# Optimization experiments

Hardware: AMD Instinct MI355X
Metric: run time of the kernel (lower is better)

The kernel has to match this reference:

```python
import jax, jax.numpy as jnp
import numpy as np

D, NH, NL, NP, DFF = 256, 8, 4, 4, 1024
HD = D // NH
SHAPES = np.array([[64, 64], [32, 32], [16, 16], [8, 8]], dtype=np.int32)  # (H, W) per level


def _layer_norm(x, g, b, eps=1e-5):
    mu = jnp.mean(x, -1, keepdims=True)
    var = jnp.mean((x - mu) ** 2, -1, keepdims=True)
    return (x - mu) * jax.lax.rsqrt(var + eps) * g + b


def _bilinear_sample(value_l, loc):
    # value_l: (N, H, W, NH, HD); loc: (N, Lq, NH, NP, 2) normalized to [0,1]
    # Matches F.grid_sample(align_corners=False, padding_mode='zeros') on grid 2*loc-1.
    N, H, W = value_l.shape[0], value_l.shape[1], value_l.shape[2]
    x = loc[..., 0] * W - 0.5
    y = loc[..., 1] * H - 0.5
    x0 = jnp.floor(x)
    y0 = jnp.floor(y)
    wx1 = x - x0
    wy1 = y - y0
    b_idx = jnp.arange(N)[:, None, None, None]
    h_idx = jnp.arange(NH)[None, None, :, None]

    def gather(yi, xi):
        valid = (yi >= 0) & (yi < H) & (xi >= 0) & (xi < W)
        yc = jnp.clip(yi, 0, H - 1).astype(jnp.int32)
        xc = jnp.clip(xi, 0, W - 1).astype(jnp.int32)
        v = value_l[b_idx, yc, xc, h_idx]  # (N, Lq, NH, NP, HD)
        return v * valid[..., None].astype(value_l.dtype)

    v00 = gather(y0, x0)
    v01 = gather(y0, x0 + 1)
    v10 = gather(y0 + 1, x0)
    v11 = gather(y0 + 1, x0 + 1)
    wx1 = wx1[..., None]
    wy1 = wy1[..., None]
    top = v00 * (1 - wx1) + v01 * wx1
    bot = v10 * (1 - wx1) + v11 * wx1
    return top * (1 - wy1) + bot * wy1  # (N, Lq, NH, NP, HD)


def setup_inputs() -> dict:
    key = jax.random.key(0)
    ks = jax.random.split(key, 24)
    N, Lq = 8, int(SHAPES.prod(axis=1).sum())  # 5440
    s = 0.02
    return {
        "src": jax.random.normal(ks[0], (N, Lq, D), jnp.float32),
        "pos": jax.random.normal(ks[1], (N, Lq, D), jnp.float32),
        "reference_points": jax.random.uniform(ks[2], (N, Lq, NL, 2), jnp.float32),
        "spatial_shapes": jnp.asarray(SHAPES),
        "W_value": s * jax.random.normal(ks[3], (D, D)),
        "b_value": jnp.zeros((D,)),
        "W_off": s * jax.random.normal(ks[4], (D, NH * NL * NP * 2)),
        "b_off": 0.5 * jax.random.normal(ks[5], (NH * NL * NP * 2,)),
        "W_attn": s * jax.random.normal(ks[6], (D, NH * NL * NP)),
        "b_attn": jnp.zeros((NH * NL * NP,)),
        "W_out": s * jax.random.normal(ks[7], (D, D)),
        "b_out": jnp.zeros((D,)),
        "ln1_g": jnp.ones((D,)),
        "ln1_b": jnp.zeros((D,)),
        "W1": s * jax.random.normal(ks[8], (D, DFF)),
        "b1": jnp.zeros((DFF,)),
        "W2": s * jax.random.normal(ks[9], (DFF, D)),
        "b2": jnp.zeros((D,)),
        "ln2_g": jnp.ones((D,)),
        "ln2_b": jnp.zeros((D,)),
    }


def reference(src, pos, reference_points, spatial_shapes,
              W_value, b_value, W_off, b_off, W_attn, b_attn, W_out, b_out,
              ln1_g, ln1_b, W1, b1, W2, b2, ln2_g, ln2_b):
    shapes = np.asarray(spatial_shapes)  # static (NL, 2)
    N, Lq = src.shape[0], src.shape[1]

    # --- MSDeformAttn ---
    query = src + pos
    value = (src @ W_value + b_value).reshape(N, Lq, NH, HD)
    offsets = (query @ W_off + b_off).reshape(N, Lq, NH, NL, NP, 2)
    attn = jax.nn.softmax((query @ W_attn + b_attn).reshape(N, Lq, NH, NL * NP), axis=-1)
    attn = attn.reshape(N, Lq, NH, NL, NP)
    # offset normalizer is (W, H) per level
    norm = jnp.asarray(np.stack([shapes[:, 1], shapes[:, 0]], -1), jnp.float32)  # (NL, 2)
    loc = reference_points[:, :, None, :, None, :] + offsets / norm[None, None, None, :, None, :]

    out = jnp.zeros((N, Lq, NH, HD), src.dtype)
    start = 0
    for l in range(NL):
        H, W = int(shapes[l, 0]), int(shapes[l, 1])
        v_l = jax.lax.dynamic_slice_in_dim(value, start, H * W, axis=1).reshape(N, H, W, NH, HD)
        sampled = _bilinear_sample(v_l, loc[:, :, :, l])  # (N, Lq, NH, NP, HD)
        out = out + jnp.einsum('nqhp,nqhpd->nqhd', attn[:, :, :, l], sampled)
        start += H * W
    src2 = out.reshape(N, Lq, D) @ W_out + b_out

    # --- residual + norm + FFN (dropout=0, eval) ---
    x = _layer_norm(src + src2, ln1_g, ln1_b)
    ffn = jax.nn.relu(x @ W1 + b1) @ W2 + b2
    return _layer_norm(x + ffn, ln2_g, ln2_b)
```

## Files before the change

### kernel.cpp

```cpp
#include <hip/hip_runtime.h>
#include <math.h>

#define LQ_ 5440
#define NB_ 8
#define NQ_ (NB_ * LQ_)
#define D_  256
#define NH_ 8
#define HD_ 32

typedef __attribute__((ext_vector_type(8))) short short8;
typedef __attribute__((ext_vector_type(4))) float f32x4;

__device__ __forceinline__ ushort f2bf(float f) {
    union { float f; unsigned u; } v; v.f = f;
    unsigned u = v.u;
    unsigned r = (u + 0x7FFFu + ((u >> 16) & 1u)) >> 16;
    return (ushort)r;
}

__device__ __forceinline__ void gload_lds16(const void* g, void* l) {
    __builtin_amdgcn_global_load_lds(
        (const __attribute__((address_space(1))) void*)g,
        (__attribute__((address_space(3))) void*)l, 16, 0, 0);
}

__device__ __forceinline__ void wg_barrier() {
    __builtin_amdgcn_sched_barrier(0);
    __builtin_amdgcn_s_barrier();
    __builtin_amdgcn_sched_barrier(0);
}

#define TPREP_ 736

__global__ __launch_bounds__(256)
void prep(const float* __restrict__ src, const float* __restrict__ pos,
          ushort* __restrict__ s_bf, ushort* __restrict__ q_bf,
          const float* __restrict__ Wv, const float* __restrict__ Woff,
          const float* __restrict__ Wattn, const float* __restrict__ Wout,
          const float* __restrict__ W1, const float* __restrict__ W2,
          ushort* __restrict__ Wv_t, ushort* __restrict__ Woff_t,
          ushort* __restrict__ Wattn_t, ushort* __restrict__ Wout_t,
          ushort* __restrict__ W1_t, ushort* __restrict__ W2_t) {
    __shared__ float tile[32][33];
    const int bid = blockIdx.x;
    const int tid = threadIdx.x;

    if (bid >= TPREP_) {
        const int i = (bid - TPREP_) * 256 + tid;
        const float4 s = ((const float4*)src)[i];
        const float4 p = ((const float4*)pos)[i];
        ushort4 a, b;
        a.x = f2bf(s.x); a.y = f2bf(s.y); a.z = f2bf(s.z); a.w = f2bf(s.w);
        b.x = f2bf(s.x + p.x); b.y = f2bf(s.y + p.y);
        b.z = f2bf(s.z + p.z); b.w = f2bf(s.w + p.w);
        ((ushort4*)s_bf)[i] = a;
        ((ushort4*)q_bf)[i] = b;
        return;
    }

    const float* W; ushort* Wt; int K, N, bx, by;
    if (bid < 64)       { W = Wv;    Wt = Wv_t;    K = 256;  N = 256;  bx = bid % 8;         by = bid / 8; }
    else if (bid < 128) { W = Woff;  Wt = Woff_t;  K = 256;  N = 256;  bx = (bid-64) % 8;    by = (bid-64) / 8; }
    else if (bid < 160) { W = Wattn; Wt = Wattn_t; K = 256;  N = 128;  bx = (bid-128) % 4;   by = (bid-128) / 4; }
    else if (bid < 224) { W = Wout;  Wt = Wout_t;  K = 256;  N = 256;  bx = (bid-160) % 8;   by = (bid-160) / 8; }
    else if (bid < 480) { W = W1;    Wt = W1_t;    K = 256;  N = 1024; bx = (bid-224) % 32;  by = (bid-224) / 32; }
    else                { W = W2;    Wt = W2_t;    K = 1024; N = 256;  bx = (bid-480) % 8;   by = (bid-480) / 8; }

    const int tx = tid & 31;
    const int ty = tid >> 5;
    for (int i = ty; i < 32; i += 8)
        tile[i][tx] = W[(size_t)(by * 32 + i) * N + bx * 32 + tx];
    __syncthreads();
    for (int i = ty; i < 32; i += 8)
        Wt[(size_t)(bx * 32 + i) * K + by * 32 + tx] = f2bf(tile[tx][i]);
}

#define BM 128
#define BN 128
#define BK 64

__global__ __launch_bounds__(256)
void mfma_gemm(const ushort* __restrict__ A, const ushort* __restrict__ Bt,
               const float* __restrict__ bias, float* __restrict__ Cf,
               ushort* __restrict__ Cb, int N, int K, int relu) {
    __shared__ ushort lA[2][BM * BK];
    __shared__ ushort lB[2][BN * BK];
    const int t = threadIdx.x;

    const int nt   = gridDim.x;
    const int nwg  = nt * gridDim.y;
    const int flat = blockIdx.y * nt + blockIdx.x;
    const int xc   = flat & 7;
    const int sl   = flat >> 3;
    const int q8   = nwg >> 3;
    const int rm8  = nwg & 7;
    const int wi   = (xc < rm8 ? xc * (q8 + 1) : rm8 * (q8 + 1) + (xc - rm8) * q8) + sl;
    const int col0 = (wi % nt) * BN;
    const int row0 = (wi / nt) * BM;

    const int w    = t >> 6;
    const int lr   = t & 15;
    const int quad = (t >> 4) & 3;
    const int wm   = (w >> 1) * 64;
    const int wn   = (w & 1) * 64;

    f32x4 acc[4][4];
    #pragma unroll
    for (int i = 0; i < 4; ++i)
        #pragma unroll
        for (int j = 0; j < 4; ++j)
            acc[i][j] = (f32x4){0.f, 0.f, 0.f, 0.f};

    const int sr = t >> 3;
    const int sc = (t & 7) * 8;
    const size_t aoff = (size_t)(row0 + sr) * K + sc;
    const size_t boff = (size_t)(col0 + sr) * K + sc;
    const int wb = w * 1024;

    auto stage = [&](int buf, int k0) {
        char* la = (char*)lA[buf] + wb;
        char* lb = (char*)lB[buf] + wb;
        #pragma unroll
        for (int g = 0; g < 4; ++g) {
            gload_lds16(A  + aoff + k0 + (size_t)g * 32 * K, la + g * 4096);
            gload_lds16(Bt + boff + k0 + (size_t)g * 32 * K, lb + g * 4096);
        }
    };

    stage(0, 0);
    int cur = 0;
    for (int k0 = 0; k0 < K; k0 += BK) {
        if (k0 + BK < K) {
            stage(cur ^ 1, k0 + BK);
            asm volatile("s_waitcnt vmcnt(8)" ::: "memory");
        } else {
            asm volatile("s_waitcnt vmcnt(0)" ::: "memory");
        }
        wg_barrier();
        const ushort* pA = lA[cur];
        const ushort* pB = lB[cur];
        #pragma unroll
        for (int kk = 0; kk < 2; ++kk) {
            short8 af[4], bfr[4];
            #pragma unroll
            for (int i = 0; i < 4; ++i)
                af[i] = *(const short8*)(pA + (wm + i * 16 + lr) * BK + kk * 32 + quad * 8);
            #pragma unroll
            for (int j = 0; j < 4; ++j)
                bfr[j] = *(const short8*)(pB + (wn + j * 16 + lr) * BK + kk * 32 + quad * 8);
            #pragma unroll
            for (int i = 0; i < 4; ++i)
                #pragma unroll
                for (int j = 0; j < 4; ++j)
                    acc[i][j] = __builtin_amdgcn_mfma_f32_16x16x32_bf16(af[i], bfr[j], acc[i][j], 0, 0, 0);
        }
        wg_barrier();
        cur ^= 1;
    }

    #pragma unroll
    for (int j = 0; j < 4; ++j) {
        const int col = col0 + wn + j * 16 + lr;
        const float bb = bias ? bias[col] : 0.f;
        #pragma unroll
        for (int i = 0; i < 4; ++i) {
            const int rbase = row0 + wm + i * 16 + quad * 4;
            #pragma unroll
            for (int r = 0; r < 4; ++r) {
                float v = acc[i][j][r] + bb;
                if (relu) v = fmaxf(v, 0.f);
                if (Cf) Cf[(size_t)(rbase + r) * N + col] = v;
                else    Cb[(size_t)(rbase + r) * N + col] = f2bf(v);
            }
        }
    }
}

__global__ __launch_bounds__(256)
void msda_sample(const ushort* __restrict__ value, const float* __restrict__ comb,
                 const float* __restrict__ b_off, const float* __restrict__ b_attn,
                 const float* __restrict__ refp, ushort* __restrict__ out) {
    __shared__ int s_blob[2048];
    int*   s_addr = s_blob;
    float* s_w    = (float*)(s_blob + 1024);

    const int t   = threadIdx.x;
    const int tq  = t >> 7;
    const int u   = t & 127;
    const int bid = blockIdx.x;
    const int swz = (bid & 7) * (NQ_ / 2 / 8) + (bid >> 3);
    const int nq  = swz * 2 + tq;
    const int n   = nq / LQ_;

    {
        const int h = u >> 4;
        const int p = u & 15;
        const int l = p >> 2;

        const int starts[4] = {0, 4096, 5120, 5376};
        const int Wl = 64 >> l;

        float a = comb[(size_t)nq * 384 + 256 + u] + b_attn[u];
        float m = a;
        #pragma unroll
        for (int o = 8; o > 0; o >>= 1) m = fmaxf(m, __shfl_xor(m, o));
        float e = __expf(a - m);
        float s = e;
        #pragma unroll
        for (int o = 8; o > 0; o >>= 1) s += __shfl_xor(s, o);
        const float wgt = e / s;

        const float rx = refp[(size_t)nq * 8 + l * 2 + 0];
        const float ry = refp[(size_t)nq * 8 + l * 2 + 1];
        const float ox = comb[(size_t)nq * 384 + u * 2 + 0] + b_off[u * 2 + 0];
        const float oy = comb[(size_t)nq * 384 + u * 2 + 1] + b_off[u * 2 + 1];

        const float fw = (float)Wl;
        const float x  = (rx + ox / fw) * fw - 0.5f;
        const float y  = (ry + oy / fw) * fw - 0.5f;
        const float x0f = floorf(x), y0f = floorf(y);
        const int   x0 = (int)x0f, y0 = (int)y0f;
        const float wx1 = x - x0f, wy1 = y - y0f;
        const float wx0 = 1.f - wx1, wy0 = 1.f - wy1;

        const float xm0 = (x0 >= 0 && x0 < Wl) ? 1.f : 0.f;
        const float xm1 = (x0 + 1 >= 0 && x0 + 1 < Wl) ? 1.f : 0.f;
        const float ym0 = (y0 >= 0 && y0 < Wl) ? 1.f : 0.f;
        const float ym1 = (y0 + 1 >= 0 && y0 + 1 < Wl) ? 1.f : 0.f;

        const int x0c = min(max(x0, 0), Wl - 1);
        const int x1c = min(max(x0 + 1, 0), Wl - 1);
        const int y0c = min(max(y0, 0), Wl - 1);
        const int y1c = min(max(y0 + 1, 0), Wl - 1);

        const int base = (n * LQ_ + starts[l]) * 512 + h * 64;
        const int idx  = (tq << 7) + (p << 3) + (h ^ (p & 7));
        s_addr[idx * 4 + 0] = base + (y0c * Wl + x0c) * 512;
        s_addr[idx * 4 + 1] = base + (y0c * Wl + x1c) * 512;
        s_addr[idx * 4 + 2] = base + (y1c * Wl + x0c) * 512;
        s_addr[idx * 4 + 3] = base + (y1c * Wl + x1c) * 512;
        s_w[idx * 4 + 0] = wgt * wy0 * wx0 * ym0 * xm0;
        s_w[idx * 4 + 1] = wgt * wy0 * wx1 * ym0 * xm1;
        s_w[idx * 4 + 2] = wgt * wy1 * wx0 * ym1 * xm0;
        s_w[idx * 4 + 3] = wgt * wy1 * wx1 * ym1 * xm1;
    }
    __syncthreads();

    {
        const int h   = u >> 4;
        const int d2  = u & 15;
        const int tqb = tq << 7;
        const uint dby = (uint)(d2 * 4);
        const char* vbase = (const char*)value;

        float acc0 = 0.f, acc1 = 0.f;
        #pragma unroll 8
        for (int p = 0; p < 16; ++p) {
            const int row = tqb + (p << 3) + (h ^ (p & 7));
            const int*   ap = s_addr + row * 4;
            const float* wp = s_w    + row * 4;
            #pragma unroll
            for (int c = 0; c < 4; ++c) {
                const uint v = *(const uint*)(vbase + ((uint)ap[c] + dby));
                const float w = wp[c];
                union { uint u; float f; } lo, hi;
                lo.u = v << 16;
                hi.u = v & 0xffff0000u;
                acc0 = fmaf(lo.f, w, acc0);
                acc1 = fmaf(hi.f, w, acc1);
            }
        }
        const uint packed = (uint)f2bf(acc0) | ((uint)f2bf(acc1) << 16);
        ((uint*)out)[(size_t)nq * 128 + u] = packed;
    }
}

__global__ __launch_bounds__(256)
void add_ln(const float* __restrict__ a, const float* __restrict__ b,
            const float* __restrict__ g, const float* __restrict__ be,
            float* __restrict__ xf, ushort* __restrict__ xb) {
    const int row  = blockIdx.x * 4 + (threadIdx.x >> 6);
    const int lane = threadIdx.x & 63;
    const size_t base = (size_t)row * 256 + lane * 4;

    const float4 av = *(const float4*)(a + base);
    const float4 bv = *(const float4*)(b + base);
    float4 x;
    x.x = av.x + bv.x; x.y = av.y + bv.y; x.z = av.z + bv.z; x.w = av.w + bv.w;

    float s = x.x + x.y + x.z + x.w;
    #pragma unroll
    for (int o = 32; o > 0; o >>= 1) s += __shfl_xor(s, o);
    const float mu = s * (1.f / 256.f);

    float4 dx;
    dx.x = x.x - mu; dx.y = x.y - mu; dx.z = x.z - mu; dx.w = x.w - mu;
    float vv = dx.x * dx.x + dx.y * dx.y + dx.z * dx.z + dx.w * dx.w;
    #pragma unroll
    for (int o = 32; o > 0; o >>= 1) vv += __shfl_xor(vv, o);
    const float rstd = rsqrtf(vv * (1.f / 256.f) + 1e-5f);

    const float4 gv  = *(const float4*)(g  + lane * 4);
    const float4 bev = *(const float4*)(be + lane * 4);
    float4 y;
    y.x = dx.x * rstd * gv.x + bev.x;
    y.y = dx.y * rstd * gv.y + bev.y;
    y.z = dx.z * rstd * gv.z + bev.z;
    y.w = dx.w * rstd * gv.w + bev.w;

    *(float4*)(xf + base) = y;
    if (xb) {
        ushort4 yb;
        yb.x = f2bf(y.x); yb.y = f2bf(y.y); yb.z = f2bf(y.z); yb.w = f2bf(y.w);
        *(ushort4*)(xb + base) = yb;
    }
}

extern "C" void kernel_launch(void* const* d_in, const int* in_sizes, int n_in,
                              void* d_out, int out_size, void* d_ws, size_t ws_size,
                              hipStream_t stream) {
    const float* src     = (const float*)d_in[0];
    const float* pos     = (const float*)d_in[1];
    const float* refp    = (const float*)d_in[2];
    const float* W_value = (const float*)d_in[4];
    const float* b_value = (const float*)d_in[5];
    const float* W_off   = (const float*)d_in[6];
    const float* b_off   = (const float*)d_in[7];
    const float* W_attn  = (const float*)d_in[8];
    const float* b_attn  = (const float*)d_in[9];
    const float* W_out   = (const float*)d_in[10];
    const float* b_out   = (const float*)d_in[11];
    const float* ln1g    = (const float*)d_in[12];
    const float* ln1b    = (const float*)d_in[13];
    const float* W1      = (const float*)d_in[14];
    const float* b1      = (const float*)d_in[15];
    const float* W2      = (const float*)d_in[16];
    const float* b2      = (const float*)d_in[17];
    const float* ln2g    = (const float*)d_in[18];
    const float* ln2b    = (const float*)d_in[19];
    float* out = (float*)d_out;
    char*  ws  = (char*)d_ws;

    const size_t SZ_BF = (size_t)NQ_ * 256 * 2;
    const size_t SZ_F  = (size_t)NQ_ * 256 * 4;
    ushort* s_bf    = (ushort*)(ws);
    ushort* q_bf    = (ushort*)(ws + SZ_BF);
    ushort* val_bf  = (ushort*)(ws + 2 * SZ_BF);
    float*  comb    = (float*) (ws + 3 * SZ_BF);
    ushort* samp_bf = (ushort*)(ws + 4 * SZ_BF + SZ_F);
    ushort* h_bf    = (ushort*)(ws);
    ushort* x_bf    = (ushort*)(ws + 3 * SZ_BF + SZ_F);
    char*   wbase   = ws + 5 * SZ_BF + SZ_F;
    ushort* Wv_t    = (ushort*)(wbase);
    ushort* Woff_t  = (ushort*)(wbase + 131072);
    ushort* Wattn_t = (ushort*)(wbase + 262144);
    ushort* Wout_t  = (ushort*)(wbase + 327680);
    ushort* W1_t    = (ushort*)(wbase + 458752);
    ushort* W2_t    = (ushort*)(wbase + 983040);
    char*   fbase   = wbase + 1507328;
    float*  src2    = (float*)(fbase);
    float*  xf      = (float*)(fbase + SZ_F);

    prep<<<dim3(TPREP_ + (NQ_ * 256 / 4) / 256), 256, 0, stream>>>(
        src, pos, s_bf, q_bf, W_value, W_off, W_attn, W_out, W1, W2,
        Wv_t, Woff_t, Wattn_t, Wout_t, W1_t, W2_t);

    const int MT = NQ_ / BM;

    mfma_gemm<<<dim3(2, MT), 256, 0, stream>>>(s_bf, Wv_t, b_value, nullptr, val_bf, 256, 256, 0);
    mfma_gemm<<<dim3(3, MT), 256, 0, stream>>>(q_bf, Woff_t, nullptr, comb, nullptr, 384, 256, 0);
    msda_sample<<<dim3(NQ_ / 2), 256, 0, stream>>>(val_bf, comb, b_off, b_attn, refp, samp_bf);
    mfma_gemm<<<dim3(2, MT), 256, 0, stream>>>(samp_bf, Wout_t, b_out, src2, nullptr, 256, 256, 0);
    add_ln<<<dim3(NQ_ / 4), 256, 0, stream>>>(src, src2, ln1g, ln1b, xf, x_bf);
    mfma_gemm<<<dim3(8, MT), 256, 0, stream>>>(x_bf, W1_t, b1, nullptr, h_bf, 1024, 256, 1);
    mfma_gemm<<<dim3(2, MT), 256, 0, stream>>>(h_bf, W2_t, b2, src2, nullptr, 256, 1024, 0);
    add_ln<<<dim3(NQ_ / 4), 256, 0, stream>>>(xf, src2, ln2g, ln2b, out, nullptr);
}
```

Baseline: 487.8 us.

## Fuse value and offset/attn GEMMs into one launch with bf16 comb output

Merges the value projection and the offset/attention projection GEMMs into a single grid, where each block picks its problem from its column index. This removes one launch and balances tail blocks across both GEMMs. The combined offset/attention output is now stored as bf16 instead of fp32, halving its write and read traffic; offsets are now rounded to bf16, which costs some sampling-location precision. The sampler's LDS layout also drops the XOR swizzle for plain per-thread indexing, which may add bank conflicts.

```diff
diff --git a/kernel.cpp b/kernel.cpp
--- a/kernel.cpp
+++ b/kernel.cpp
@@ -16,6 +16,9 @@
     unsigned u = v.u;
     unsigned r = (u + 0x7FFFu + ((u >> 16) & 1u)) >> 16;
     return (ushort)r;
+}
+__device__ __forceinline__ float bf2f(ushort u) {
+    union { unsigned u; float f; } v; v.u = ((unsigned)u) << 16; return v.f;
 }
 
 __device__ __forceinline__ void gload_lds16(const void* g, void* l) {
@@ -79,25 +82,12 @@
 #define BN 128
 #define BK 64
 
-__global__ __launch_bounds__(256)
-void mfma_gemm(const ushort* __restrict__ A, const ushort* __restrict__ Bt,
-               const float* __restrict__ bias, float* __restrict__ Cf,
-               ushort* __restrict__ Cb, int N, int K, int relu) {
-    __shared__ ushort lA[2][BM * BK];
-    __shared__ ushort lB[2][BN * BK];
-    const int t = threadIdx.x;
-
-    const int nt   = gridDim.x;
-    const int nwg  = nt * gridDim.y;
-    const int flat = blockIdx.y * nt + blockIdx.x;
-    const int xc   = flat & 7;
-    const int sl   = flat >> 3;
-    const int q8   = nwg >> 3;
-    const int rm8  = nwg & 7;
-    const int wi   = (xc < rm8 ? xc * (q8 + 1) : rm8 * (q8 + 1) + (xc - rm8) * q8) + sl;
-    const int col0 = (wi % nt) * BN;
-    const int row0 = (wi / nt) * BM;
-
+__device__ __forceinline__ void gemm_body(
+    ushort* __restrict__ lAb, ushort* __restrict__ lBb,
+    const ushort* __restrict__ A, const ushort* __restrict__ Bt,
+    const float* __restrict__ bias, float* __restrict__ Cf,
+    ushort* __restrict__ Cb, int N, int K, int relu, int col0, int row0) {
+    const int t    = threadIdx.x;
     const int w    = t >> 6;
     const int lr   = t & 15;
     const int quad = (t >> 4) & 3;
@@ -118,8 +108,8 @@
     const int wb = w * 1024;
 
     auto stage = [&](int buf, int k0) {
-        char* la = (char*)lA[buf] + wb;
-        char* lb = (char*)lB[buf] + wb;
+        char* la = (char*)(lAb + buf * (BM * BK)) + wb;
+        char* lb = (char*)(lBb + buf * (BN * BK)) + wb;
         #pragma unroll
         for (int g = 0; g < 4; ++g) {
             gload_lds16(A  + aoff + k0 + (size_t)g * 32 * K, la + g * 4096);
@@ -137,8 +127,8 @@
             asm volatile("s_waitcnt vmcnt(0)" ::: "memory");
         }
         wg_barrier();
-        const ushort* pA = lA[cur];
-        const ushort* pB = lB[cur];
+        const ushort* pA = lAb + cur * (BM * BK);
+        const ushort* pB = lBb + cur * (BN * BK);
         #pragma unroll
         for (int kk = 0; kk < 2; ++kk) {
             short8 af[4], bfr[4];
@@ -177,12 +167,53 @@
 }
 
 __global__ __launch_bounds__(256)
-void msda_sample(const ushort* __restrict__ value, const float* __restrict__ comb,
+void mfma_gemm(const ushort* __restrict__ A, const ushort* __restrict__ Bt,
+               const float* __restrict__ bias, float* __restrict__ Cf,
+               ushort* __restrict__ Cb, int N, int K, int relu) {
+    __shared__ ushort lA[2][BM * BK];
+    __shared__ ushort lB[2][BN * BK];
+    const int nt   = gridDim.x;
+    const int nwg  = nt * gridDim.y;
+    const int flat = blockIdx.y * nt + blockIdx.x;
+    const int xc   = flat & 7;
+    const int sl   = flat >> 3;
+    const int q8   = nwg >> 3;
+    const int rm8  = nwg & 7;
+    const int wi   = (xc < rm8 ? xc * (q8 + 1) : rm8 * (q8 + 1) + (xc - rm8) * q8) + sl;
+    gemm_body(&lA[0][0], &lB[0][0], A, Bt, bias, Cf, Cb, N, K, relu,
+              (wi % nt) * BN, (wi / nt) * BM);
+}
+
+__global__ __launch_bounds__(256)
+void gemm_vc(const ushort* __restrict__ s_bf, const ushort* __restrict__ q_bf,
+             const ushort* __restrict__ Wv_t, const ushort* __restrict__ Woff_t,
+             const float* __restrict__ b_value,
+             ushort* __restrict__ val_bf, ushort* __restrict__ comb_bf) {
+    __shared__ ushort lA[2][BM * BK];
+    __shared__ ushort lB[2][BN * BK];
+    const int nwg  = gridDim.x;
+    const int flat = blockIdx.x;
+    const int xc   = flat & 7;
+    const int sl   = flat >> 3;
+    const int q8   = nwg >> 3;
+    const int rm8  = nwg & 7;
+    const int wi   = (xc < rm8 ? xc * (q8 + 1) : rm8 * (q8 + 1) + (xc - rm8) * q8) + sl;
+    const int ci   = wi % 5;
+    const int row0 = (wi / 5) * BM;
+    if (ci < 2)
+        gemm_body(&lA[0][0], &lB[0][0], s_bf, Wv_t, b_value, nullptr, val_bf,
+                  256, 256, 0, ci * BN, row0);
+    else
+        gemm_body(&lA[0][0], &lB[0][0], q_bf, Woff_t, nullptr, nullptr, comb_bf,
+                  384, 256, 0, (ci - 2) * BN, row0);
+}
+
+__global__ __launch_bounds__(256)
+void msda_sample(const ushort* __restrict__ value, const ushort* __restrict__ comb,
                  const float* __restrict__ b_off, const float* __restrict__ b_attn,
                  const float* __restrict__ refp, ushort* __restrict__ out) {
-    __shared__ int s_blob[2048];
-    int*   s_addr = s_blob;
-    float* s_w    = (float*)(s_blob + 1024);
+    __shared__ int   s_addr[256][4];
+    __shared__ float s_w[256][4];
 
     const int t   = threadIdx.x;
     const int tq  = t >> 7;
@@ -200,7 +231,7 @@
         const int starts[4] = {0, 4096, 5120, 5376};
         const int Wl = 64 >> l;
 
-        float a = comb[(size_t)nq * 384 + 256 + u] + b_attn[u];
+        float a = bf2f(comb[(size_t)nq * 384 + 256 + u]) + b_attn[u];
         float m = a;
         #pragma unroll
         for (int o = 8; o > 0; o >>= 1) m = fmaxf(m, __shfl_xor(m, o));
@@ -212,8 +243,9 @@
 
         const float rx = refp[(size_t)nq * 8 + l * 2 + 0];
         const float ry = refp[(size_t)nq * 8 + l * 2 + 1];
-        const float ox = comb[(size_t)nq * 384 + u * 2 + 0] + b_off[u * 2 + 0];
-        const float oy = comb[(size_t)nq * 384 + u * 2 + 1] + b_off[u * 2 + 1];
+        const uint  opk = *(const uint*)(comb + (size_t)nq * 384 + u * 2);
+        const float ox = bf2f((ushort)(opk & 0xffffu))  + b_off[u * 2 + 0];
+        const float oy = bf2f((ushort)(opk >> 16))      + b_off[u * 2 + 1];
 
         const float fw = (float)Wl;
         const float x  = (rx + ox / fw) * fw - 0.5f;
@@ -234,31 +266,29 @@
         const int y1c = min(max(y0 + 1, 0), Wl - 1);
 
         const int base = (n * LQ_ + starts[l]) * 512 + h * 64;
-        const int idx  = (tq << 7) + (p << 3) + (h ^ (p & 7));
-        s_addr[idx * 4 + 0] = base + (y0c * Wl + x0c) * 512;
-        s_addr[idx * 4 + 1] = base + (y0c * Wl + x1c) * 512;
-        s_addr[idx * 4 + 2] = base + (y1c * Wl + x0c) * 512;
-        s_addr[idx * 4 + 3] = base + (y1c * Wl + x1c) * 512;
-        s_w[idx * 4 + 0] = wgt * wy0 * wx0 * ym0 * xm0;
-        s_w[idx * 4 + 1] = wgt * wy0 * wx1 * ym0 * xm1;
-        s_w[idx * 4 + 2] = wgt * wy1 * wx0 * ym1 * xm0;
-        s_w[idx * 4 + 3] = wgt * wy1 * wx1 * ym1 * xm1;
+        s_addr[t][0] = base + (y0c * Wl + x0c) * 512;
+        s_addr[t][1] = base + (y0c * Wl + x1c) * 512;
+        s_addr[t][2] = base + (y1c * Wl + x0c) * 512;
+        s_addr[t][3] = base + (y1c * Wl + x1c) * 512;
+        s_w[t][0] = wgt * wy0 * wx0 * ym0 * xm0;
+        s_w[t][1] = wgt * wy0 * wx1 * ym0 * xm1;
+        s_w[t][2] = wgt * wy1 * wx0 * ym1 * xm0;
+        s_w[t][3] = wgt * wy1 * wx1 * ym1 * xm1;
     }
     __syncthreads();
 
     {
         const int h   = u >> 4;
         const int d2  = u & 15;
-        const int tqb = tq << 7;
+        const int sb  = tq * 128 + h * 16;
         const uint dby = (uint)(d2 * 4);
         const char* vbase = (const char*)value;
 
         float acc0 = 0.f, acc1 = 0.f;
         #pragma unroll 8
         for (int p = 0; p < 16; ++p) {
-            const int row = tqb + (p << 3) + (h ^ (p & 7));
-            const int*   ap = s_addr + row * 4;
-            const float* wp = s_w    + row * 4;
+            const int*   ap = s_addr[sb + p];
+            const float* wp = s_w[sb + p];
             #pragma unroll
             for (int c = 0; c < 4; ++c) {
                 const uint v = *(const uint*)(vbase + ((uint)ap[c] + dby));
@@ -341,16 +371,17 @@
     float* out = (float*)d_out;
     char*  ws  = (char*)d_ws;
 
-    const size_t SZ_BF = (size_t)NQ_ * 256 * 2;
-    const size_t SZ_F  = (size_t)NQ_ * 256 * 4;
+    const size_t SZ_BF  = (size_t)NQ_ * 256 * 2;
+    const size_t SZ_CB  = (size_t)NQ_ * 384 * 2;
+    const size_t SZ_F   = (size_t)NQ_ * 256 * 4;
     ushort* s_bf    = (ushort*)(ws);
     ushort* q_bf    = (ushort*)(ws + SZ_BF);
     ushort* val_bf  = (ushort*)(ws + 2 * SZ_BF);
-    float*  comb    = (float*) (ws + 3 * SZ_BF);
-    ushort* samp_bf = (ushort*)(ws + 4 * SZ_BF + SZ_F);
+    ushort* comb    = (ushort*)(ws + 3 * SZ_BF);
+    ushort* samp_bf = (ushort*)(ws + 3 * SZ_BF + SZ_CB);
     ushort* h_bf    = (ushort*)(ws);
-    ushort* x_bf    = (ushort*)(ws + 3 * SZ_BF + SZ_F);
-    char*   wbase   = ws + 5 * SZ_BF + SZ_F;
+    ushort* x_bf    = (ushort*)(ws + 3 * SZ_BF + SZ_CB);
+    char*   wbase   = ws + 3 * SZ_BF + SZ_CB + SZ_BF;
     ushort* Wv_t    = (ushort*)(wbase);
     ushort* Woff_t  = (ushort*)(wbase + 131072);
     ushort* Wattn_t = (ushort*)(wbase + 262144);
@@ -367,8 +398,7 @@
 
     const int MT = NQ_ / BM;
 
-    mfma_gemm<<<dim3(2, MT), 256, 0, stream>>>(s_bf, Wv_t, b_value, nullptr, val_bf, 256, 256, 0);
-    mfma_gemm<<<dim3(3, MT), 256, 0, stream>>>(q_bf, Woff_t, nullptr, comb, nullptr, 384, 256, 0);
+    gemm_vc<<<dim3(5 * MT), 256, 0, stream>>>(s_bf, q_bf, Wv_t, Woff_t, b_value, val_bf, comb);
     msda_sample<<<dim3(NQ_ / 2), 256, 0, stream>>>(val_bf, comb, b_off, b_attn, refp, samp_bf);
     mfma_gemm<<<dim3(2, MT), 256, 0, stream>>>(samp_bf, Wout_t, b_out, src2, nullptr, 256, 256, 0);
     add_ln<<<dim3(NQ_ / 4), 256, 0, stream>>>(src, src2, ln1g, ln1b, xf, x_bf);
```

Result: faster. 440.0 us (-9.8%).
